# Kernel tuning notes

Hardware: AMD Instinct MI355X
Metric: run time of the kernel (lower is better)

## Reference

```python
import jax, jax.numpy as jnp
import numpy as np

E = 5        # num_experts
K = 2        # top-k routing
DIM = 768    # token dim
HID = 3072   # dim * mlp_ratio
T = 16384    # num tokens (batch*seq collapsed, per SparseDispatcher contract)
EPS = float(np.finfo(np.float64).eps)  # np.finfo(float).eps used in combine


def setup_inputs() -> dict:
    key = jax.random.key(0)
    ks = jax.random.split(key, 5)
    x = jax.random.normal(ks[0], (T, DIM), jnp.float32)
    # w_gate is nn.Parameter(zeros) in the source; randomize so routing is non-trivial
    w_gate = jax.random.normal(ks[1], (DIM, E), jnp.float32) * 0.02
    # stacked ExpertMLP params (fc1: dim->hid, fc2: hid->dim), small init per init_weights
    W1 = jax.random.normal(ks[2], (E, DIM, HID), jnp.float32) * 0.02
    b1 = jnp.zeros((E, HID), jnp.float32)
    W2 = jax.random.normal(ks[3], (E, HID, DIM), jnp.float32) * 0.02
    b2 = jnp.zeros((E, DIM), jnp.float32)
    return {"x": x, "w_gate": w_gate, "W1": W1, "b1": b1, "W2": W2, "b2": b2}


def reference(x, w_gate, W1, b1, W2, b2):
    # --- noisy top-k gating, eval mode (no noise added at inference) ---
    logits = x @ w_gate                              # [T, E]
    top_vals, top_idx = jax.lax.top_k(logits, K)     # [T, K]
    top_gates = jax.nn.softmax(top_vals, axis=-1)    # softmax over selected logits
    tok = jnp.arange(x.shape[0])[:, None]
    gates = jnp.zeros_like(logits).at[tok, top_idx].set(top_gates)  # sparse [T, E]

    # --- dispatch / expert MLP / combine ---
    # SparseDispatcher.combine: combined[b] = log(sum_e gate[b,e] * exp(expert_e(x[b])))
    # (zeros where no expert contributes are replaced by eps before log)
    acc = jnp.zeros((x.shape[0], DIM), jnp.float32)
    for e in range(E):  # small fixed expert count; dense-equivalent of sparse dispatch
        h = jax.nn.gelu(x @ W1[e] + b1[e], approximate=False)  # torch nn.GELU (erf)
        y = h @ W2[e] + b2[e]                                   # [T, DIM]
        acc = acc + gates[:, e:e + 1] * jnp.exp(y)
    return jnp.log(jnp.where(acc == 0.0, EPS, acc))
```

## Files before the change

### kernel.cpp

```cpp
#include <hip/hip_runtime.h>
#include <math.h>

#define T_TOK 16384
#define DIM   768
#define HID   3072
#define NE    5
#define MT    65
#define HCAP  (MT * 128)
#define CSTR  32
#define EPSF  2.2204460492503131e-16f
#define NXCD  8

typedef short bf16x8  __attribute__((ext_vector_type(8)));
typedef float f32x4   __attribute__((ext_vector_type(4)));
typedef float f32x16  __attribute__((ext_vector_type(16)));

#define MFMA16(A, B, C) __builtin_amdgcn_mfma_f32_16x16x32_bf16((A), (B), (C), 0, 0, 0)
#define MFMA32(A, B, C) __builtin_amdgcn_mfma_f32_32x32x16_bf16((A), (B), (C), 0, 0, 0)

__device__ __forceinline__ unsigned short f2bf(float f) {
    unsigned int u = __float_as_uint(f);
    unsigned int r = (u + 0x7fffu + ((u >> 16) & 1u)) >> 16;
    return (unsigned short)r;
}

__device__ __forceinline__ void gld16(const void* g, void* l) {
    __builtin_amdgcn_global_load_lds(
        (const __attribute__((address_space(1))) void*)g,
        (__attribute__((address_space(3))) void*)l, 16, 0, 0);
}

__global__ void prep_w1p(const float* __restrict__ W1, unsigned short* __restrict__ W1p) {
    int idx = blockIdx.x * 256 + threadIdx.x;
    if (idx >= NE * 24 * 12 * 128 * 8) return;
    int p = idx & 7;
    int n = (idx >> 3) & 127;
    int t = idx >> 10;
    int kb = t % 12; t /= 12;
    int nb = t % 24; int e = t / 24;
    int klog = kb * 64 + (p ^ (n & 7)) * 8;
    const float* src = W1 + ((size_t)e * DIM + klog) * HID + nb * 128 + n;
    bf16x8 v;
    #pragma unroll
    for (int j = 0; j < 8; ++j) v[j] = (short)f2bf(src[(size_t)j * HID]);
    *reinterpret_cast<bf16x8*>(W1p + (size_t)idx * 8) = v;
}

__global__ void prep_w2p(const float* __restrict__ W2, unsigned short* __restrict__ W2p) {
    int idx = blockIdx.x * 256 + threadIdx.x;
    if (idx >= NE * 6 * 48 * 128 * 8) return;
    int p = idx & 7;
    int n = (idx >> 3) & 127;
    int t = idx >> 10;
    int kb = t % 48; t /= 48;
    int nb = t % 6; int e = t / 6;
    int klog = kb * 64 + (p ^ (n & 7)) * 8;
    const float* src = W2 + ((size_t)e * HID + klog) * DIM + nb * 128 + n;
    bf16x8 v;
    #pragma unroll
    for (int j = 0; j < 8; ++j) v[j] = (short)f2bf(src[(size_t)j * DIM]);
    *reinterpret_cast<bf16x8*>(W2p + (size_t)idx * 8) = v;
}

__global__ __launch_bounds__(256) void gate_kernel(
    const float* __restrict__ x, const float* __restrict__ wg,
    unsigned short* __restrict__ xb, int* __restrict__ counts,
    int* __restrict__ btok, float* __restrict__ bgate) {
    __shared__ int   s_e[2][64];
    __shared__ float s_g[2][64];
    __shared__ int   lcnt[NE];
    __shared__ int   gbase[NE];

    const int tid = threadIdx.x;
    if (tid < NE) lcnt[tid] = 0;
    const int grp = tid >> 4, l16 = tid & 15;
    const int t0 = blockIdx.x * 64 + grp * 4;

    double acc[4][NE];
    #pragma unroll
    for (int tt = 0; tt < 4; ++tt)
        #pragma unroll
        for (int e = 0; e < NE; ++e) acc[tt][e] = 0.0;

    for (int i = 0; i < 12; ++i) {
        const int dbase = i * 64 + l16 * 4;
        float4 xv[4];
        #pragma unroll
        for (int tt = 0; tt < 4; ++tt) {
            xv[tt] = *reinterpret_cast<const float4*>(x + (size_t)(t0 + tt) * DIM + dbase);
            ushort4 o;
            o.x = f2bf(xv[tt].x); o.y = f2bf(xv[tt].y);
            o.z = f2bf(xv[tt].z); o.w = f2bf(xv[tt].w);
            *reinterpret_cast<ushort4*>(xb + (size_t)(t0 + tt) * DIM + dbase) = o;
        }
        #pragma unroll
        for (int j = 0; j < 4; ++j) {
            const int d = dbase + j;
            float w0 = wg[d * NE + 0], w1 = wg[d * NE + 1], w2 = wg[d * NE + 2];
            float w3 = wg[d * NE + 3], w4 = wg[d * NE + 4];
            #pragma unroll
            for (int tt = 0; tt < 4; ++tt) {
                double xd = (double)((&xv[tt].x)[j]);
                acc[tt][0] += xd * (double)w0;
                acc[tt][1] += xd * (double)w1;
                acc[tt][2] += xd * (double)w2;
                acc[tt][3] += xd * (double)w3;
                acc[tt][4] += xd * (double)w4;
            }
        }
    }
    #pragma unroll
    for (int off = 8; off; off >>= 1)
        #pragma unroll
        for (int tt = 0; tt < 4; ++tt)
            #pragma unroll
            for (int e = 0; e < NE; ++e)
                acc[tt][e] += __shfl_down(acc[tt][e], off, 16);

    if (l16 == 0) {
        #pragma unroll
        for (int tt = 0; tt < 4; ++tt) {
            double v[NE] = {acc[tt][0], acc[tt][1], acc[tt][2], acc[tt][3], acc[tt][4]};
            int i0 = 0;
            for (int e = 1; e < NE; ++e) if (v[e] > v[i0]) i0 = e;
            int i1 = -1;
            for (int e = 0; e < NE; ++e) {
                if (e == i0) continue;
                if (i1 < 0 || v[e] > v[i1]) i1 = e;
            }
            float e1 = expf((float)(v[i1] - v[i0]));
            float g0 = 1.0f / (1.0f + e1);
            int li = grp * 4 + tt;
            s_e[0][li] = i0;  s_g[0][li] = g0;
            s_e[1][li] = i1;  s_g[1][li] = e1 * g0;
        }
    }
    __syncthreads();

    int mye = 0, myoff = 0, mytok = 0;
    float myg = 0.0f;
    if (tid < 128) {
        int li = tid >> 1, which = tid & 1;
        mye = s_e[which][li];
        myg = s_g[which][li];
        mytok = blockIdx.x * 64 + li;
        myoff = atomicAdd(&lcnt[mye], 1);
    }
    __syncthreads();
    if (tid < NE) gbase[tid] = atomicAdd(&counts[tid * CSTR], lcnt[tid]);
    __syncthreads();
    if (tid < 128) {
        int p = gbase[mye] + myoff;
        btok[mye * T_TOK + p] = mytok;
        bgate[mye * T_TOK + p] = myg;
    }
}

__global__ __launch_bounds__(256, 4) void combo_kernel(
    const unsigned short* __restrict__ xb,
    const unsigned short* __restrict__ W1p,
    const unsigned short* __restrict__ W2p,
    const float* __restrict__ b1, const float* __restrict__ b2,
    const int* __restrict__ counts, const int* __restrict__ btok,
    const float* __restrict__ bgate,
    unsigned short* __restrict__ h0, unsigned short* __restrict__ h1,
    float* __restrict__ out, int g1e, int g2e) {
    __shared__ __align__(16) unsigned short As[128 * 64];
    __shared__ __align__(16) unsigned short Bs[128 * 64];
    __shared__ int   sst[128];
    __shared__ float ssg[128];

    const int x = blockIdx.x & 7;
    const int i = blockIdx.x >> 3;
    const int NG2 = (g2e >= 0) ? MT : 0;
    const int NG1 = (g1e >= 0) ? MT : 0;
    const int n2x = (x < NG2) ? (((NG2 - 1 - x) >> 3) + 1) : 0;
    const int n1x = (x < NG1) ? (((NG1 - 1 - x) >> 3) + 1) : 0;
    bool isG2; int e, mt, nt;
    if (i < n2x * 6) {
        isG2 = true;  e = g2e; mt = x + 8 * (i / 6);  nt = i % 6;
    } else {
        int ii = i - n2x * 6;
        if (ii >= n1x * 24) return;
        isG2 = false; e = g1e; mt = x + 8 * (ii / 24); nt = ii % 24;
    }
    const int cnt = counts[e * CSTR];
    const int m0 = mt * 128;
    if (m0 >= cnt) return;
    unsigned short* hbuf = (e & 1) ? h1 : h0;

    const int tid = threadIdx.x;
    const int wv = tid >> 6, lane = tid & 63;
    const int wm = wv >> 1, wn = wv & 1;
    const int col = lane & 15, quad = lane >> 4;
    const int l8 = lane & 7, r8 = lane >> 3;

    const unsigned short* aptr[4];
    if (isG2) {
        if (tid < 128) {
            int pos = m0 + tid;
            sst[tid] = (pos < cnt) ? btok[e * T_TOK + pos] : 0;
            ssg[tid] = (pos < cnt) ? bgate[e * T_TOK + pos] : 0.0f;
        }
        #pragma unroll
        for (int q = 0; q < 4; ++q) {
            int r = wv * 32 + q * 8 + r8;
            aptr[q] = hbuf + (size_t)(m0 + r) * HID + (l8 ^ r8) * 8;
        }
    } else {
        #pragma unroll
        for (int q = 0; q < 4; ++q) {
            int r = wv * 32 + q * 8 + r8;
            int pos = m0 + r;
            int tok = btok[e * T_TOK + (pos < cnt ? pos : 0)];
            aptr[q] = xb + (size_t)tok * DIM + (l8 ^ r8) * 8;
        }
    }
    const unsigned short* btile = isG2
        ? W2p + ((size_t)(e * 6 + nt)) * 48 * 8192
        : W1p + ((size_t)(e * 24 + nt)) * 12 * 8192;
    const int ksteps = isG2 ? 48 : 12;

    f32x4 acc[4][4];
    #pragma unroll
    for (int i2 = 0; i2 < 4; ++i2)
        #pragma unroll
        for (int j = 0; j < 4; ++j)
            acc[i2][j] = (f32x4){0.f, 0.f, 0.f, 0.f};

    for (int ks = 0; ks < ksteps; ++ks) {
        const unsigned short* bk = btile + (size_t)ks * 8192 + (size_t)wv * 2048 + lane * 8;
        #pragma unroll
        for (int q = 0; q < 4; ++q)
            gld16(aptr[q] + ks * 64, &As[(wv * 4 + q) * 512]);
        #pragma unroll
        for (int q = 0; q < 4; ++q)
            gld16(bk + q * 512, &Bs[(wv * 4 + q) * 512]);
        __syncthreads();
        #pragma unroll
        for (int kf = 0; kf < 2; ++kf) {
            const int p = ((kf * 4 + quad) ^ l8) * 8;
            bf16x8 a[4], b[4];
            #pragma unroll
            for (int i2 = 0; i2 < 4; ++i2)
                a[i2] = *reinterpret_cast<const bf16x8*>(&As[(wm * 64 + i2 * 16 + col) * 64 + p]);
            #pragma unroll
            for (int i2 = 0; i2 < 4; ++i2)
                b[i2] = *reinterpret_cast<const bf16x8*>(&Bs[(wn * 64 + i2 * 16 + col) * 64 + p]);
            #pragma unroll
            for (int i2 = 0; i2 < 4; ++i2)
                #pragma unroll
                for (int j = 0; j < 4; ++j)
                    acc[i2][j] = MFMA16(a[i2], b[j], acc[i2][j]);
        }
        __syncthreads();
    }

    const int nb0 = nt * 128 + wn * 64;
    if (!isG2) {
        #pragma unroll
        for (int j = 0; j < 4; ++j) {
            float bias = b1[e * HID + nb0 + j * 16 + col];
            #pragma unroll
            for (int i2 = 0; i2 < 4; ++i2) {
                #pragma unroll
                for (int r = 0; r < 4; ++r) {
                    int row = m0 + wm * 64 + i2 * 16 + quad * 4 + r;
                    float v = acc[i2][j][r] + bias;
                    float gl = 0.5f * v * (1.0f + erff(v * 0.70710678118654752f));
                    hbuf[(size_t)row * HID + nb0 + j * 16 + col] = f2bf(gl);
                }
            }
        }
    } else {
        #pragma unroll
        for (int j = 0; j < 4; ++j) {
            float bias = b2[e * DIM + nb0 + j * 16 + col];
            #pragma unroll
            for (int i2 = 0; i2 < 4; ++i2) {
                #pragma unroll
                for (int r = 0; r < 4; ++r) {
                    int lrow = wm * 64 + i2 * 16 + quad * 4 + r;
                    float g = ssg[lrow];
                    if (g > 0.0f) {
                        float v = acc[i2][j][r] + bias;
                        atomicAdd(out + (size_t)sst[lrow] * DIM + nb0 + j * 16 + col,
                                  g * expf(v));
                    }
                }
            }
        }
    }
}

__global__ void log_kernel(float* __restrict__ out, int n4) {
    int i = blockIdx.x * 256 + threadIdx.x;
    if (i < n4) {
        float4 v = reinterpret_cast<float4*>(out)[i];
        v.x = logf(v.x == 0.0f ? EPSF : v.x);
        v.y = logf(v.y == 0.0f ? EPSF : v.y);
        v.z = logf(v.z == 0.0f ? EPSF : v.z);
        v.w = logf(v.w == 0.0f ? EPSF : v.w);
        reinterpret_cast<float4*>(out)[i] = v;
    }
}

__global__ void prep_w1_v2(const float* __restrict__ W1, unsigned short* __restrict__ W1s) {
    int g = blockIdx.x * 4 + (threadIdx.x >> 6);
    int lane = threadIdx.x & 63;
    int kf = g % 48;
    int rest = g / 48;
    int nt2 = rest % 96;
    int e = rest / 96;
    int n = nt2 * 32 + (lane & 31);
    int k0 = kf * 16 + (lane >> 5) * 8;
    const float* src = W1 + ((size_t)e * DIM + k0) * HID + n;
    bf16x8 v;
    #pragma unroll
    for (int j = 0; j < 8; ++j) v[j] = (short)f2bf(src[(size_t)j * HID]);
    *reinterpret_cast<bf16x8*>(W1s + ((size_t)g * 64 + lane) * 8) = v;
}

__global__ void prep_w2_v2(const float* __restrict__ W2, unsigned short* __restrict__ W2s) {
    int g = blockIdx.x * 4 + (threadIdx.x >> 6);
    int lane = threadIdx.x & 63;
    int kf = g % 192;
    int rest = g / 192;
    int nt2 = rest % 24;
    int e = rest / 24;
    int n = nt2 * 32 + (lane & 31);
    int k0 = kf * 16 + (lane >> 5) * 8;
    const float* src = W2 + ((size_t)e * HID + k0) * DIM + n;
    bf16x8 v;
    #pragma unroll
    for (int j = 0; j < 8; ++j) v[j] = (short)f2bf(src[(size_t)j * DIM]);
    *reinterpret_cast<bf16x8*>(W2s + ((size_t)g * 64 + lane) * 8) = v;
}

__global__ __launch_bounds__(512, 2) void expert_v2(
    const unsigned short* __restrict__ xb, const unsigned short* __restrict__ W1s,
    const unsigned short* __restrict__ W2s, const float* __restrict__ b1,
    const float* __restrict__ b2, const int* __restrict__ counts,
    const int* __restrict__ btok, const float* __restrict__ bgate,
    float* __restrict__ out) {
    __shared__ __align__(16) unsigned short xs[64][776];
    __shared__ __align__(16) unsigned short hs[2][64][136];
    __shared__ int   st[64];
    __shared__ float sg[64];

    const int e = blockIdx.y;
    const int cnt = counts[e * CSTR];
    const int m0 = blockIdx.x * 64;
    if (m0 >= cnt) return;

    const int tid = threadIdx.x;
    const int wv = tid >> 6, lane = tid & 63;
    const int l31 = lane & 31, lhi = lane >> 5;

    if (tid < 64) {
        int pos = m0 + tid;
        st[tid] = (pos < cnt) ? btok[e * T_TOK + pos] : 0;
        sg[tid] = (pos < cnt) ? bgate[e * T_TOK + pos] : 0.0f;
    }
    __syncthreads();
    {
        int r = tid >> 3, seg = tid & 7;
        const unsigned short* src = xb + (size_t)st[r] * DIM + seg * 96;
        unsigned short* dst = &xs[r][seg * 96];
        #pragma unroll
        for (int i = 0; i < 12; ++i)
            reinterpret_cast<bf16x8*>(dst)[i] = reinterpret_cast<const bf16x8*>(src)[i];
    }
    __syncthreads();

    const int mt2 = wv & 1, nt2l = wv >> 1;
    f32x16 acc[2][3];
    #pragma unroll
    for (int a_ = 0; a_ < 2; ++a_)
        #pragma unroll
        for (int b_ = 0; b_ < 3; ++b_)
            #pragma unroll
            for (int q = 0; q < 16; ++q) acc[a_][b_][q] = 0.0f;

    const unsigned short* arow = &xs[mt2 * 32 + l31][lhi * 8];
    for (int jc = 0; jc < 24; ++jc) {
        f32x16 c0, c1;
        #pragma unroll
        for (int q = 0; q < 16; ++q) { c0[q] = 0.0f; c1[q] = 0.0f; }
        const unsigned short* bpa =
            W1s + ((size_t)((e * 96 + jc * 4 + nt2l) * 48)) * 512 + lane * 8;
        #pragma unroll
        for (int kf = 0; kf < 48; kf += 2) {
            bf16x8 a0 = *reinterpret_cast<const bf16x8*>(arow + kf * 16);
            bf16x8 b0 = *reinterpret_cast<const bf16x8*>(bpa + (size_t)kf * 512);
            c0 = MFMA32(a0, b0, c0);
            bf16x8 a1 = *reinterpret_cast<const bf16x8*>(arow + kf * 16 + 16);
            bf16x8 b1 = *reinterpret_cast<const bf16x8*>(bpa + (size_t)kf * 512 + 512);
            c1 = MFMA32(a1, b1, c1);
        }
        #pragma unroll
        for (int q = 0; q < 16; ++q) c0[q] += c1[q];
        {
            int colc = nt2l * 32 + l31;
            float bias = b1[e * HID + jc * 128 + colc];
            #pragma unroll
            for (int reg = 0; reg < 16; ++reg) {
                int row = (reg & 3) + 8 * (reg >> 2) + 4 * lhi;
                float v = c0[reg] + bias;
                float gl = 0.5f * v * (1.0f + erff(v * 0.70710678118654752f));
                hs[jc & 1][mt2 * 32 + row][colc] = f2bf(gl);
            }
        }
        __syncthreads();
        const unsigned short* bpb =
            W2s + ((size_t)((e * 24 + wv * 3) * 192 + jc * 8)) * 512 + lane * 8;
        #pragma unroll
        for (int kf = 0; kf < 8; ++kf) {
            bf16x8 af0 = *reinterpret_cast<const bf16x8*>(&hs[jc & 1][l31][kf * 16 + lhi * 8]);
            bf16x8 af1 = *reinterpret_cast<const bf16x8*>(&hs[jc & 1][32 + l31][kf * 16 + lhi * 8]);
            #pragma unroll
            for (int i = 0; i < 3; ++i) {
                bf16x8 bv = *reinterpret_cast<const bf16x8*>(bpb + ((size_t)i * 192 + kf) * 512);
                acc[0][i] = MFMA32(af0, bv, acc[0][i]);
                acc[1][i] = MFMA32(af1, bv, acc[1][i]);
            }
        }
    }
    #pragma unroll
    for (int mt = 0; mt < 2; ++mt) {
        #pragma unroll
        for (int i = 0; i < 3; ++i) {
            int cg = (wv * 3 + i) * 32 + l31;
            float bias2 = b2[e * DIM + cg];
            #pragma unroll
            for (int reg = 0; reg < 16; ++reg) {
                int row = mt * 32 + (reg & 3) + 8 * (reg >> 2) + 4 * lhi;
                float g = sg[row];
                if (g > 0.0f) {
                    float v = acc[mt][i][reg] + bias2;
                    atomicAdd(out + (size_t)st[row] * DIM + cg, g * expf(v));
                }
            }
        }
    }
}


extern "C" void kernel_launch(void* const* d_in, const int* in_sizes, int n_in,
                              void* d_out, int out_size, void* d_ws, size_t ws_size,
                              hipStream_t stream) {
    const float* x  = (const float*)d_in[0];
    const float* wg = (const float*)d_in[1];
    const float* W1 = (const float*)d_in[2];
    const float* b1 = (const float*)d_in[3];
    const float* W2 = (const float*)d_in[4];
    const float* b2 = (const float*)d_in[5];
    float* out = (float*)d_out;

    char* ws = (char*)d_ws;
    int*            counts = (int*)ws;
    int*            btok   = (int*)(ws + 1024);
    float*          bgate  = (float*)(ws + 1024 + 327680);
    unsigned short* xb     = (unsigned short*)(ws + 1024 + 2 * 327680);
    unsigned short* W1b    = xb + (size_t)T_TOK * DIM;
    unsigned short* W2b    = W1b + (size_t)NE * DIM * HID;
    unsigned short* h0     = W2b + (size_t)NE * HID * DIM;
    unsigned short* h1     = h0 + (size_t)HCAP * HID;

    const size_t need_fast = 1024 + 2 * 327680
        + (size_t)T_TOK * DIM * 2 + 2 * (size_t)NE * DIM * HID * 2
        + 2 * (size_t)HCAP * HID * 2;
    const bool fast = ws_size >= need_fast;

    hipMemsetAsync(counts, 0, 1024, stream);
    hipMemsetAsync(out, 0, (size_t)out_size * sizeof(float), stream);

    gate_kernel<<<T_TOK / 64, 256, 0, stream>>>(x, wg, xb, counts, btok, bgate);

    if (fast) {
        prep_w1p<<<(NE * 24 * 12 * 128 * 8 + 255) / 256, 256, 0, stream>>>(W1, W1b);
        prep_w2p<<<(NE * 6 * 48 * 128 * 8 + 255) / 256, 256, 0, stream>>>(W2, W2b);
        const int gmax = (MT + 7) / 8;
        for (int s = 0; s < 6; ++s) {
            int g1e = (s <= 4) ? s : -1;
            int g2e = s - 1;
            int per_x0 = (g2e >= 0 ? gmax * 6 : 0) + (g1e >= 0 ? gmax * 24 : 0);
            combo_kernel<<<NXCD * per_x0, 256, 0, stream>>>(
                xb, W1b, W2b, b1, b2, counts, btok, bgate, h0, h1, out, g1e, g2e);
        }
    } else {
        prep_w1_v2<<<NE * 96 * 48 / 4, 256, 0, stream>>>(W1, W1b);
        prep_w2_v2<<<NE * 24 * 192 / 4, 256, 0, stream>>>(W2, W2b);
        expert_v2<<<dim3(T_TOK / 64, NE), 512, 0, stream>>>(
            xb, W1b, W2b, b1, b2, counts, btok, bgate, out);
    }

    log_kernel<<<(out_size / 4 + 255) / 256, 256, 0, stream>>>(out, out_size / 4);
}
```

Measured before the change: 799.2 us.

## Replace atomic accumulation with plain stores into two partial buffers

The gate sign now encodes whether a token's expert slot is its first or second choice. The second-layer epilogue writes g*exp(y) with plain stores, first choices to out and second choices to a separate p1 buffer, instead of doing atomicAdd into out. A new log2 kernel sums the two partials before taking the log, and the memset of out is skipped because each element is written by exactly one slot per buffer. This removes atomic traffic and the memset, at the cost of an extra 48MB buffer and an extra read in the final pass. It relies on every token writing both slots, including zero-gate ones.

Measured after the change: 720.7 us, median of 2. 9.8% less time.

```diff
diff --git a/kernel.cpp b/kernel.cpp
--- a/kernel.cpp
+++ b/kernel.cpp
@@ -132,7 +132,7 @@
             float g0 = 1.0f / (1.0f + e1);
             int li = grp * 4 + tt;
             s_e[0][li] = i0;  s_g[0][li] = g0;
-            s_e[1][li] = i1;  s_g[1][li] = e1 * g0;
+            s_e[1][li] = i1;  s_g[1][li] = -(e1 * g0);
         }
     }
     __syncthreads();
@@ -164,7 +164,7 @@
     const int* __restrict__ counts, const int* __restrict__ btok,
     const float* __restrict__ bgate,
     unsigned short* __restrict__ h0, unsigned short* __restrict__ h1,
-    float* __restrict__ out, int g1e, int g2e) {
+    float* __restrict__ out, float* __restrict__ p1, int g1e, int g2e) {
     __shared__ __align__(16) unsigned short As[128 * 64];
     __shared__ __align__(16) unsigned short Bs[128 * 64];
     __shared__ int   sst[128];
@@ -199,7 +199,7 @@
     if (isG2) {
         if (tid < 128) {
             int pos = m0 + tid;
-            sst[tid] = (pos < cnt) ? btok[e * T_TOK + pos] : 0;
+            sst[tid] = (pos < cnt) ? btok[e * T_TOK + pos] : -1;
             ssg[tid] = (pos < cnt) ? bgate[e * T_TOK + pos] : 0.0f;
         }
         #pragma unroll
@@ -281,11 +281,19 @@
                 #pragma unroll
                 for (int r = 0; r < 4; ++r) {
                     int lrow = wm * 64 + i2 * 16 + quad * 4 + r;
-                    float g = ssg[lrow];
-                    if (g > 0.0f) {
+                    int tok = sst[lrow];
+                    if (tok >= 0) {
+                        float graw = ssg[lrow];
+                        float g = fabsf(graw);
                         float v = acc[i2][j][r] + bias;
-                        atomicAdd(out + (size_t)sst[lrow] * DIM + nb0 + j * 16 + col,
-                                  g * expf(v));
+                        size_t off = (size_t)tok * DIM + nb0 + j * 16 + col;
+                        if (p1) {
+                            float val = (g > 0.0f) ? g * expf(v) : 0.0f;
+                            float* dst = (__float_as_uint(graw) >> 31) ? p1 : out;
+                            dst[off] = val;
+                        } else if (g > 0.0f) {
+                            atomicAdd(out + off, g * expf(v));
+                        }
                     }
                 }
             }
@@ -302,6 +310,20 @@
         v.z = logf(v.z == 0.0f ? EPSF : v.z);
         v.w = logf(v.w == 0.0f ? EPSF : v.w);
         reinterpret_cast<float4*>(out)[i] = v;
+    }
+}
+
+__global__ void log2_kernel(float* __restrict__ out, const float* __restrict__ p1, int n4) {
+    int i = blockIdx.x * 256 + threadIdx.x;
+    if (i < n4) {
+        float4 a = reinterpret_cast<float4*>(out)[i];
+        float4 b = reinterpret_cast<const float4*>(p1)[i];
+        float sx = a.x + b.x, sy = a.y + b.y, sz = a.z + b.z, sw = a.w + b.w;
+        a.x = logf(sx == 0.0f ? EPSF : sx);
+        a.y = logf(sy == 0.0f ? EPSF : sy);
+        a.z = logf(sz == 0.0f ? EPSF : sz);
+        a.w = logf(sw == 0.0f ? EPSF : sw);
+        reinterpret_cast<float4*>(out)[i] = a;
     }
 }
 
@@ -360,7 +382,7 @@
     if (tid < 64) {
         int pos = m0 + tid;
         st[tid] = (pos < cnt) ? btok[e * T_TOK + pos] : 0;
-        sg[tid] = (pos < cnt) ? bgate[e * T_TOK + pos] : 0.0f;
+        sg[tid] = (pos < cnt) ? fabsf(bgate[e * T_TOK + pos]) : 0.0f;
     }
     __syncthreads();
     {
@@ -466,34 +488,42 @@
     unsigned short* W2b    = W1b + (size_t)NE * DIM * HID;
     unsigned short* h0     = W2b + (size_t)NE * HID * DIM;
     unsigned short* h1     = h0 + (size_t)HCAP * HID;
+    float*          p1     = (float*)(h1 + (size_t)HCAP * HID);
 
     const size_t need_fast = 1024 + 2 * 327680
         + (size_t)T_TOK * DIM * 2 + 2 * (size_t)NE * DIM * HID * 2
         + 2 * (size_t)HCAP * HID * 2;
-    const bool fast = ws_size >= need_fast;
+    const size_t need_store = need_fast + (size_t)T_TOK * DIM * 4;
+    const bool fast  = ws_size >= need_fast;
+    const bool store = ws_size >= need_store;
 
     hipMemsetAsync(counts, 0, 1024, stream);
-    hipMemsetAsync(out, 0, (size_t)out_size * sizeof(float), stream);
+    if (!(fast && store))
+        hipMemsetAsync(out, 0, (size_t)out_size * sizeof(float), stream);
 
     gate_kernel<<<T_TOK / 64, 256, 0, stream>>>(x, wg, xb, counts, btok, bgate);
 
     if (fast) {
         prep_w1p<<<(NE * 24 * 12 * 128 * 8 + 255) / 256, 256, 0, stream>>>(W1, W1b);
         prep_w2p<<<(NE * 6 * 48 * 128 * 8 + 255) / 256, 256, 0, stream>>>(W2, W2b);
+        float* p1arg = store ? p1 : nullptr;
         const int gmax = (MT + 7) / 8;
         for (int s = 0; s < 6; ++s) {
             int g1e = (s <= 4) ? s : -1;
             int g2e = s - 1;
             int per_x0 = (g2e >= 0 ? gmax * 6 : 0) + (g1e >= 0 ? gmax * 24 : 0);
             combo_kernel<<<NXCD * per_x0, 256, 0, stream>>>(
-                xb, W1b, W2b, b1, b2, counts, btok, bgate, h0, h1, out, g1e, g2e);
-        }
+                xb, W1b, W2b, b1, b2, counts, btok, bgate, h0, h1, out, p1arg, g1e, g2e);
+        }
+        if (store)
+            log2_kernel<<<(out_size / 4 + 255) / 256, 256, 0, stream>>>(out, p1, out_size / 4);
+        else
+            log_kernel<<<(out_size / 4 + 255) / 256, 256, 0, stream>>>(out, out_size / 4);
     } else {
         prep_w1_v2<<<NE * 96 * 48 / 4, 256, 0, stream>>>(W1, W1b);
         prep_w2_v2<<<NE * 24 * 192 / 4, 256, 0, stream>>>(W2, W2b);
         expert_v2<<<dim3(T_TOK / 64, NE), 512, 0, stream>>>(
             xb, W1b, W2b, b1, b2, counts, btok, bgate, out);
-    }
-
-    log_kernel<<<(out_size / 4 + 255) / 256, 256, 0, stream>>>(out, out_size / 4);
-}
+        log_kernel<<<(out_size / 4 + 255) / 256, 256, 0, stream>>>(out, out_size / 4);
+    }
+}
```
